# Performance work log

Measured on AMD Instinct MI355X. Metric: run time of the kernel, lower is better.

The kernel has to match this reference:

```python
import jax, jax.numpy as jnp
import numpy as np

N0, P1 = 10000, 30000
N1 = N0 + P1            # 40000
P2 = 120000
N2 = N1 + P2            # 160000
E0, E1, E2 = 60000, 120000, 480000
IN, H, OUT, K = 3, 192, 3, 2


def setup_inputs() -> dict:
    key = jax.random.key(0)
    k = jax.random.split(key, 13)
    return {
        "features": jax.random.normal(k[0], (N0, IN), jnp.float32),
        "src0": jax.random.randint(k[1], (E0,), 0, N0, jnp.int32),
        "dst0": jax.random.randint(k[2], (E0,), 0, N0, jnp.int32),
        "pool_idx0": jax.random.randint(k[3], (P1, 2), 0, N0, jnp.int32),
        "edge0": jax.random.randint(k[4], (E1, 2), 0, N1, jnp.int32),
        "pool_idx1": jax.random.randint(k[5], (P2, 2), 0, N1, jnp.int32),
        "edge1": jax.random.randint(k[6], (E2, 2), 0, N2, jnp.int32),
        "W_first": 0.3 * jax.random.normal(k[7], (3, (K + 1) * IN, H), jnp.float32),
        "b_first": jnp.zeros((3, H), jnp.float32),
        "W_mid": 0.04 * jax.random.normal(k[8], (3, 12, (K + 1) * H, H), jnp.float32),
        "b_mid": jnp.zeros((3, 12, H), jnp.float32),
        "W_last": 0.05 * jax.random.normal(k[9], (3, (K + 1) * H, OUT), jnp.float32),
        "b_last": jnp.zeros((3, OUT), jnp.float32),
    }


def _norm(dst, n):
    # symmetric-norm factor D^{-1/2}, degrees clamped at 1 (DGL TAGConv)
    deg = jax.ops.segment_sum(jnp.ones(dst.shape[0], jnp.float32), dst, num_segments=n)
    return jnp.clip(deg, 1.0) ** -0.5  # [n]


def _tagconv(x, src, dst, n, norm, W, b):
    fs = [x]
    h = x
    for _ in range(K):
        h = norm[:, None] * jax.ops.segment_sum((h * norm[:, None])[src], dst, num_segments=n)
        fs.append(h)
    return jnp.concatenate(fs, axis=1) @ W + b


def _stage(x, src, dst, n, Wf, bf, Wm, bm, Wl, bl):
    norm = _norm(dst, n)
    h = jax.nn.relu(_tagconv(x, src, dst, n, norm, Wf, bf))
    prev = h  # raw output of previous layer (hidden[-2] in the torch code)
    for i in range(12):
        cur = jax.nn.relu(_tagconv(h, src, dst, n, norm, Wm[i], bm[i]))
        h = 0.5 * (prev + cur) if (i + 1) in (2, 4, 6, 8, 10, 12) else cur
        prev = cur
    return _tagconv(h, src, dst, n, norm, Wl, bl)  # identity activation


def _unpool(feat, pool_idx):
    # new vertex = midpoint of its two parents; appended to the node table
    new_vs = 0.5 * (feat[pool_idx[:, 0]] + feat[pool_idx[:, 1]])
    return jnp.concatenate([feat, new_vs], axis=0)


def _bidir(edge):
    # graph.add_edges(src, dst); graph.add_edges(dst, src)
    return (jnp.concatenate([edge[:, 0], edge[:, 1]]),
            jnp.concatenate([edge[:, 1], edge[:, 0]]))


def reference(features, src0, dst0, pool_idx0, edge0, pool_idx1, edge1,
              W_first, b_first, W_mid, b_mid, W_last, b_last):
    out1 = _stage(features, src0, dst0, N0,
                  W_first[0], b_first[0], W_mid[0], b_mid[0], W_last[0], b_last[0])
    h = _unpool(out1, pool_idx0)            # [N1, 3]
    out1_2 = h
    s1, d1 = _bidir(edge0)
    out2 = _stage(h, s1, d1, N1,
                  W_first[1], b_first[1], W_mid[1], b_mid[1], W_last[1], b_last[1])
    h = _unpool(out2, pool_idx1)            # [N2, 3]
    out2_2 = h
    s2, d2 = _bidir(edge1)
    out3 = _stage(h, s2, d2, N2,
                  W_first[2], b_first[2], W_mid[2], b_mid[2], W_last[2], b_last[2])
    return (out1, out2, out3, out1_2, out2_2)
```

## Files before the change

kernel.cpp:

```cpp
#include <hip/hip_runtime.h>
#include <hip/hip_fp16.h>

#define HF 192

static inline int divup(int a, int b){ return (a+b-1)/b; }

typedef _Float16 half8 __attribute__((ext_vector_type(8)));
typedef float f32x4 __attribute__((ext_vector_type(4)));

#define G_WS_BYTES 195734272ull
__device__ __align__(256) char g_ws[G_WS_BYTES];

#define OFF_HH    0ull
#define OFF_T1H   61440000ull
#define OFF_T2H   122880000ull
#define OFF_DEG  184320000ull
#define OFF_RP   184960000ull
#define OFF_COL  185600032ull
#define OFF_NRM  189440032ull
#define OFF_O1F  190080032ull
#define OFF_U1F  190200032ull
#define OFF_O2F  190680032ull
#define OFF_U2F  191160032ull
#define OFF_WT   193080032ull
#define OFF_X1F  OFF_T1H
#define OFF_X2F  (OFF_T1H + 1920000ull)

__device__ __forceinline__ float*  wsf(unsigned long long o){ return (float*) (g_ws + o); }
__device__ __forceinline__ int*    wsi(unsigned long long o){ return (int*)   (g_ws + o); }
__device__ __forceinline__ __half* wsh(unsigned long long o){ return (__half*)(g_ws + o); }

__global__ void k_zero(unsigned long long off, int n) {
  int i = blockIdx.x*blockDim.x + threadIdx.x;
  if (i < n) wsi(off)[i] = 0;
}
__global__ void k_copyi(unsigned long long aOff, unsigned long long bOff, int n) {
  int i = blockIdx.x*blockDim.x + threadIdx.x;
  if (i < n) wsi(bOff)[i] = wsi(aOff)[i];
}

__global__ void k_count_direct(const int* __restrict__ dst, int E) {
  int* deg = wsi(OFF_DEG);
  int e = blockIdx.x*blockDim.x + threadIdx.x;
  if (e < E) atomicAdd(&deg[dst[e]], 1);
}
__global__ void k_count_bidir(const int* __restrict__ edge, int E) {
  int* deg = wsi(OFF_DEG);
  int e = blockIdx.x*blockDim.x + threadIdx.x;
  if (e < E) {
    atomicAdd(&deg[edge[2*e+1]], 1);
    atomicAdd(&deg[edge[2*e  ]], 1);
  }
}
__global__ void k_norm(int n) {
  const int* deg = wsi(OFF_DEG);
  float* nrm = wsf(OFF_NRM);
  int i = blockIdx.x*blockDim.x + threadIdx.x;
  if (i < n) {
    int d = deg[i]; if (d < 1) d = 1;
    nrm[i] = rsqrtf((float)d);
  }
}
__global__ __launch_bounds__(1024) void k_exscan(int n) {
  const int* in = wsi(OFF_DEG);
  int* out = wsi(OFF_RP);
  __shared__ int sm[1024];
  int t = threadIdx.x;
  int carry = 0;
  for (int base = 0; base < n; base += 4096) {
    int idx = base + t*4;
    int v0 = (idx+0 < n) ? in[idx+0] : 0;
    int v1 = (idx+1 < n) ? in[idx+1] : 0;
    int v2 = (idx+2 < n) ? in[idx+2] : 0;
    int v3 = (idx+3 < n) ? in[idx+3] : 0;
    int s = v0+v1+v2+v3;
    sm[t] = s;
    __syncthreads();
    for (int off = 1; off < 1024; off <<= 1) {
      int u = (t >= off) ? sm[t-off] : 0;
      __syncthreads();
      sm[t] += u;
      __syncthreads();
    }
    int excl = carry + sm[t] - s;
    if (idx   < n) out[idx]   = excl;
    if (idx+1 < n) out[idx+1] = excl + v0;
    if (idx+2 < n) out[idx+2] = excl + v0+v1;
    if (idx+3 < n) out[idx+3] = excl + v0+v1+v2;
    carry += sm[1023];
    __syncthreads();
  }
  if (t == 0) out[n] = carry;
}
__global__ void k_fill_direct(const int* __restrict__ src, const int* __restrict__ dst, int E) {
  int* cur = wsi(OFF_DEG);
  int* col = wsi(OFF_COL);
  int e = blockIdx.x*blockDim.x + threadIdx.x;
  if (e < E) {
    int p = atomicAdd(&cur[dst[e]], 1);
    col[p] = src[e];
  }
}
__global__ void k_fill_bidir(const int* __restrict__ edge, int E) {
  int* cur = wsi(OFF_DEG);
  int* col = wsi(OFF_COL);
  int e = blockIdx.x*blockDim.x + threadIdx.x;
  if (e < E) {
    int u = edge[2*e], v = edge[2*e+1];
    int p = atomicAdd(&cur[v], 1); col[p] = u;
    int q = atomicAdd(&cur[u], 1); col[q] = v;
  }
}

__global__ void k_spmm3(const float* __restrict__ Xext, unsigned long long Xoff,
                        unsigned long long Yoff, int n) {
  const float* X = Xext ? Xext : wsf(Xoff);
  float* Y = wsf(Yoff);
  const int* rowptr = wsi(OFF_RP);
  const int* col = wsi(OFF_COL);
  const float* nrm = wsf(OFF_NRM);
  int row = blockIdx.x*blockDim.x + threadIdx.x;
  if (row >= n) return;
  int s = rowptr[row], e = rowptr[row+1];
  float a0=0.f, a1=0.f, a2=0.f;
  for (int i = s; i < e; ++i) {
    int c = col[i]; float v = nrm[c];
    a0 = fmaf(v, X[c*3+0], a0);
    a1 = fmaf(v, X[c*3+1], a1);
    a2 = fmaf(v, X[c*3+2], a2);
  }
  float nm = nrm[row];
  Y[row*3+0] = a0*nm; Y[row*3+1] = a1*nm; Y[row*3+2] = a2*nm;
}

__global__ __launch_bounds__(192) void k_spmm8(unsigned long long Xoff,
                                               unsigned long long Yoff, int n) {
  int gid = blockIdx.x*192 + threadIdx.x;
  if (gid >= n*24) return;
  int row = gid / 24, f8 = gid - row*24;
  const half8* __restrict__ X8 = (const half8*)wsh(Xoff);
  half8* __restrict__ Y8 = (half8*)wsh(Yoff);
  const int* rowptr = wsi(OFF_RP);
  const int* col = wsi(OFF_COL);
  const float* nrm = wsf(OFF_NRM);
  int s = rowptr[row], e = rowptr[row+1];
  float acc0[8], acc1[8];
  #pragma unroll
  for (int j = 0; j < 8; ++j) { acc0[j] = 0.f; acc1[j] = 0.f; }
  int i = s;
  for (; i + 4 <= e; i += 4) {
    int c0 = col[i], c1 = col[i+1], c2 = col[i+2], c3 = col[i+3];
    float w0 = nrm[c0], w1 = nrm[c1], w2 = nrm[c2], w3 = nrm[c3];
    half8 v0 = X8[(size_t)c0*24 + f8];
    half8 v1 = X8[(size_t)c1*24 + f8];
    half8 v2 = X8[(size_t)c2*24 + f8];
    half8 v3 = X8[(size_t)c3*24 + f8];
    #pragma unroll
    for (int j = 0; j < 8; ++j) {
      acc0[j] = fmaf(w0, (float)v0[j], acc0[j]);
      acc1[j] = fmaf(w1, (float)v1[j], acc1[j]);
      acc0[j] = fmaf(w2, (float)v2[j], acc0[j]);
      acc1[j] = fmaf(w3, (float)v3[j], acc1[j]);
    }
  }
  for (; i + 2 <= e; i += 2) {
    int c0 = col[i], c1 = col[i+1];
    float w0 = nrm[c0], w1 = nrm[c1];
    half8 v0 = X8[(size_t)c0*24 + f8];
    half8 v1 = X8[(size_t)c1*24 + f8];
    #pragma unroll
    for (int j = 0; j < 8; ++j) {
      acc0[j] = fmaf(w0, (float)v0[j], acc0[j]);
      acc1[j] = fmaf(w1, (float)v1[j], acc1[j]);
    }
  }
  if (i < e) {
    int c0 = col[i];
    float w0 = nrm[c0];
    half8 v0 = X8[(size_t)c0*24 + f8];
    #pragma unroll
    for (int j = 0; j < 8; ++j) acc0[j] = fmaf(w0, (float)v0[j], acc0[j]);
  }
  float nm = nrm[row];
  half8 r;
  #pragma unroll
  for (int j = 0; j < 8; ++j) r[j] = (_Float16)((acc0[j] + acc1[j])*nm);
  Y8[(size_t)row*24 + f8] = r;
}

__global__ void k_gemm_first(const float* __restrict__ xext, unsigned long long xOff,
                             const float* __restrict__ W, const float* __restrict__ b, int n) {
  const float* x  = xext ? xext : wsf(xOff);
  const float* x1 = wsf(OFF_X1F);
  const float* x2 = wsf(OFF_X2F);
  __half* H = wsh(OFF_HH);
  int idx = blockIdx.x*blockDim.x + threadIdx.x;
  if (idx >= n*HF) return;
  int row = idx / HF, c = idx - row*HF;
  float acc = b[c];
  #pragma unroll
  for (int k = 0; k < 3; ++k) acc = fmaf(x [row*3+k], W[(0+k)*HF + c], acc);
  #pragma unroll
  for (int k = 0; k < 3; ++k) acc = fmaf(x1[row*3+k], W[(3+k)*HF + c], acc);
  #pragma unroll
  for (int k = 0; k < 3; ++k) acc = fmaf(x2[row*3+k], W[(6+k)*HF + c], acc);
  H[idx] = __float2half(fmaxf(acc, 0.f));
}

__global__ void k_wprep(const float* __restrict__ Wm, int s) {
  int idx = blockIdx.x*blockDim.x + threadIdx.x;
  if (idx >= 12*576*HF) return;
  int it = idx / (576*HF);
  int rem = idx - it*576*HF;
  int k = rem / HF;
  int c = rem - k*HF;
  wsh(OFF_WT)[(size_t)it*HF*576 + (size_t)c*576 + k] =
      __float2half(Wm[((size_t)(s*12+it)*576 + k)*HF + c]);
}

#define BPAD 104
__global__ __launch_bounds__(256) void k_mfma_mid(
    const float* __restrict__ b, int it, int n, int residual)
{
  __half* __restrict__ H = wsh(OFF_HH);
  const __half* __restrict__ T1 = wsh(OFF_T1H);
  const __half* __restrict__ T2 = wsh(OFF_T2H);
  const __half* __restrict__ Wt = wsh(OFF_WT) + (size_t)it*HF*576;
  __shared__ _Float16 Bs[192*BPAD];
  int t = threadIdx.x;
  int w = t >> 6;
  int l = t & 63;
  int lr = l & 15;
  int lg = l >> 4;
  int row0 = blockIdx.x*64 + w*16;

  f32x4 acc[12];
  #pragma unroll
  for (int i = 0; i < 12; ++i) acc[i] = (f32x4){0.f,0.f,0.f,0.f};

  const __half* Xp[3] = { H, T1, T2 };
  for (int p = 0; p < 3; ++p) {
    const __half* X = Xp[p];
    half8 a[6];
    #pragma unroll
    for (int q = 0; q < 6; ++q)
      a[q] = *(const half8*)&X[(size_t)(row0 + lr)*HF + q*32 + lg*8];
    for (int kh = 0; kh < 2; ++kh) {
      __syncthreads();
      for (int i = t; i < 192*12; i += 256) {
        int c  = i / 12;
        int k8 = i - c*12;
        *(half8*)&Bs[c*BPAD + k8*8] =
            *(const half8*)&Wt[(size_t)c*576 + p*HF + kh*96 + k8*8];
      }
      __syncthreads();
      #pragma unroll
      for (int k0i = 0; k0i < 3; ++k0i) {
        half8 av = a[kh*3 + k0i];
        #pragma unroll
        for (int tl = 0; tl < 12; ++tl) {
          half8 bb = *(const half8*)&Bs[(tl*16 + lr)*BPAD + k0i*32 + lg*8];
          acc[tl] = __builtin_amdgcn_mfma_f32_16x16x32_f16(av, bb, acc[tl], 0, 0, 0);
        }
      }
    }
  }

  #pragma unroll
  for (int tl = 0; tl < 12; ++tl) {
    int c = tl*16 + lr;
    float bias = b[c];
    #pragma unroll
    for (int j = 0; j < 4; ++j) {
      int row = row0 + lg*4 + j;
      if (row < n) {
        size_t o = (size_t)row*HF + c;
        float cur = fmaxf(acc[tl][j] + bias, 0.f);
        float h = cur;
        if (residual) h = 0.5f*(__half2float(H[o]) + cur);
        H[o] = __float2half(h);
      }
    }
  }
}

__global__ void k_last_lin(const float* __restrict__ W, const float* __restrict__ b,
                           float* __restrict__ outb, unsigned long long outfOff,
                           int hasOutf, int n) {
  int row = blockIdx.x*blockDim.x + threadIdx.x;
  if (row >= n) return;
  const __half* bufs[3] = { wsh(OFF_HH), wsh(OFF_T1H), wsh(OFF_T2H) };
  float a0 = b[0], a1 = b[1], a2 = b[2];
  for (int p = 0; p < 3; ++p) {
    const half8* x8 = (const half8*)&bufs[p][(size_t)row*HF];
    #pragma unroll 4
    for (int k8 = 0; k8 < 24; ++k8) {
      half8 v = x8[k8];
      #pragma unroll
      for (int j = 0; j < 8; ++j) {
        int k = k8*8 + j;
        const float* w = &W[(p*HF + k)*3];
        float vv = (float)v[j];
        a0 = fmaf(vv, w[0], a0); a1 = fmaf(vv, w[1], a1); a2 = fmaf(vv, w[2], a2);
      }
    }
  }
  outb[row*3+0] = a0;
  outb[row*3+1] = a1;
  outb[row*3+2] = a2;
  if (hasOutf) {
    float* outf = wsf(outfOff);
    outf[row*3+0] = a0; outf[row*3+1] = a1; outf[row*3+2] = a2;
  }
}

__global__ void k_unpool(unsigned long long srcOff, const int* __restrict__ pidx,
                         unsigned long long dstfOff, float* __restrict__ dstb,
                         int n, int P) {
  const float* src = wsf(srcOff);
  float* dstf = wsf(dstfOff);
  int i = blockIdx.x*blockDim.x + threadIdx.x;
  if (i >= n + P) return;
  float v0, v1, v2;
  if (i < n) {
    v0 = src[i*3+0]; v1 = src[i*3+1]; v2 = src[i*3+2];
  } else {
    int a = pidx[(i-n)*2], c = pidx[(i-n)*2+1];
    v0 = 0.5f*(src[a*3+0] + src[c*3+0]);
    v1 = 0.5f*(src[a*3+1] + src[c*3+1]);
    v2 = 0.5f*(src[a*3+2] + src[c*3+2]);
  }
  dstf[i*3+0] = v0; dstf[i*3+1] = v1; dstf[i*3+2] = v2;
  dstb[i*3+0] = v0;
  dstb[i*3+1] = v1;
  dstb[i*3+2] = v2;
}

extern "C" void kernel_launch(void* const* d_in, const int* in_sizes, int n_in,
                              void* d_out, int out_size, void* d_ws, size_t ws_size,
                              hipStream_t stream) {
  (void)in_sizes; (void)n_in; (void)out_size; (void)d_ws; (void)ws_size;
  const float* features = (const float*)d_in[0];
  const int*  src0  = (const int*)d_in[1];
  const int*  dst0  = (const int*)d_in[2];
  const int*  pool0 = (const int*)d_in[3];
  const int*  edge0 = (const int*)d_in[4];
  const int*  pool1 = (const int*)d_in[5];
  const int*  edge1 = (const int*)d_in[6];
  const float* Wf = (const float*)d_in[7];
  const float* bfp = (const float*)d_in[8];
  const float* Wm = (const float*)d_in[9];
  const float* bm = (const float*)d_in[10];
  const float* Wl = (const float*)d_in[11];
  const float* bl = (const float*)d_in[12];
  float* out = (float*)d_out;

  auto csr = [&](int n, const int* srcD, const int* dstD, int Edir,
                 const int* edgeB, int Eund) {
    k_zero<<<divup(n,256),256,0,stream>>>(OFF_DEG, n);
    if (srcD) k_count_direct<<<divup(Edir,256),256,0,stream>>>(dstD, Edir);
    else      k_count_bidir <<<divup(Eund,256),256,0,stream>>>(edgeB, Eund);
    k_norm<<<divup(n,256),256,0,stream>>>(n);
    k_exscan<<<1,1024,0,stream>>>(n);
    k_copyi<<<divup(n,256),256,0,stream>>>(OFF_RP, OFF_DEG, n);
    if (srcD) k_fill_direct<<<divup(Edir,256),256,0,stream>>>(srcD, dstD, Edir);
    else      k_fill_bidir<<<divup(Eund,256),256,0,stream>>>(edgeB, Eund);
  };

  auto stage_u = [&](const float* xext, unsigned long long xOff, int n,
                     const int* srcD, const int* dstD, int Edir,
                     const int* edgeB, int Eund,
                     int s, float* outb, unsigned long long outfOff, int hasOutf) {
    csr(n, srcD, dstD, Edir, edgeB, Eund);
    k_wprep<<<divup(12*576*HF,256),256,0,stream>>>(Wm, s);
    k_spmm3<<<divup(n,256),256,0,stream>>>(xext, xOff, OFF_X1F, n);
    k_spmm3<<<divup(n,256),256,0,stream>>>(nullptr, OFF_X1F, OFF_X2F, n);
    k_gemm_first<<<divup(n*HF,256),256,0,stream>>>(xext, xOff,
        Wf + (size_t)s*9*HF, bfp + s*HF, n);
    int gsp = divup(n*24,192);
    for (int it = 0; it < 12; ++it) {
      k_spmm8<<<gsp,192,0,stream>>>(OFF_HH,  OFF_T1H, n);
      k_spmm8<<<gsp,192,0,stream>>>(OFF_T1H, OFF_T2H, n);
      k_mfma_mid<<<divup(n,64),256,0,stream>>>(bm + (s*12+it)*HF, it, n,
          ((it+1)%2==0) ? 1 : 0);
    }
    k_spmm8<<<gsp,192,0,stream>>>(OFF_HH,  OFF_T1H, n);
    k_spmm8<<<gsp,192,0,stream>>>(OFF_T1H, OFF_T2H, n);
    k_last_lin<<<divup(n,256),256,0,stream>>>(Wl + (size_t)s*576*3, bl + s*3,
        outb, outfOff, hasOutf, n);
  };

  stage_u(features, 0ull, 10000, src0, dst0, 60000, nullptr, 0,
          0, out + 0, OFF_O1F, 1);
  k_unpool<<<divup(40000,256),256,0,stream>>>(OFF_O1F, pool0, OFF_U1F, out + 630000, 10000, 30000);
  stage_u(nullptr, OFF_U1F, 40000, nullptr, nullptr, 0, edge0, 120000,
          1, out + 30000, OFF_O2F, 1);
  k_unpool<<<divup(160000,256),256,0,stream>>>(OFF_O2F, pool1, OFF_U2F, out + 750000, 40000, 120000);
  stage_u(nullptr, OFF_U2F, 160000, nullptr, nullptr, 0, edge1, 480000,
          2, out + 150000, OFF_O1F, 0);
}
```

Before: 5.833 ms.

## Switch mid-layer GEMM to 32x32x16 MFMA tiles with 128-row blocks

The mid-layer TAGConv GEMM moves from 16x16x32 MFMA tiles (16 rows per wave) to 32x32x16 tiles (32 rows per wave, 128 rows per block). Each weight tile staged in shared memory is now reused across twice as many rows, which halves the per-row LDS B-fragment traffic and the number of blocks that restage the weights. A fragments are now loaded from global memory inside the k loop instead of being preloaded, and the epilogue uses the 32x32 accumulator row mapping. A min-blocks occupancy hint is also added, which may limit registers given the 96-float accumulator per lane.

After: 5.757 ms. About the same (-1.3%).

```diff
diff --git a/kernel.cpp b/kernel.cpp
--- a/kernel.cpp
+++ b/kernel.cpp
@@ -7,6 +7,7 @@
 
 typedef _Float16 half8 __attribute__((ext_vector_type(8)));
 typedef float f32x4 __attribute__((ext_vector_type(4)));
+typedef float f32x16 __attribute__((ext_vector_type(16)));
 
 #define G_WS_BYTES 195734272ull
 __device__ __align__(256) char g_ws[G_WS_BYTES];
@@ -219,7 +220,7 @@
 }
 
 #define BPAD 104
-__global__ __launch_bounds__(256) void k_mfma_mid(
+__global__ __launch_bounds__(256,4) void k_mfma_mid(
     const float* __restrict__ b, int it, int n, int residual)
 {
   __half* __restrict__ H = wsh(OFF_HH);
@@ -230,21 +231,19 @@
   int t = threadIdx.x;
   int w = t >> 6;
   int l = t & 63;
-  int lr = l & 15;
-  int lg = l >> 4;
-  int row0 = blockIdx.x*64 + w*16;
-
-  f32x4 acc[12];
-  #pragma unroll
-  for (int i = 0; i < 12; ++i) acc[i] = (f32x4){0.f,0.f,0.f,0.f};
+  int lc = l & 31;
+  int lg = l >> 5;
+  int rowW = blockIdx.x*128 + w*32;
+
+  f32x16 acc[6];
+  #pragma unroll
+  for (int i = 0; i < 6; ++i)
+    #pragma unroll
+    for (int r = 0; r < 16; ++r) acc[i][r] = 0.f;
 
   const __half* Xp[3] = { H, T1, T2 };
   for (int p = 0; p < 3; ++p) {
     const __half* X = Xp[p];
-    half8 a[6];
-    #pragma unroll
-    for (int q = 0; q < 6; ++q)
-      a[q] = *(const half8*)&X[(size_t)(row0 + lr)*HF + q*32 + lg*8];
     for (int kh = 0; kh < 2; ++kh) {
       __syncthreads();
       for (int i = t; i < 192*12; i += 256) {
@@ -255,27 +254,28 @@
       }
       __syncthreads();
       #pragma unroll
-      for (int k0i = 0; k0i < 3; ++k0i) {
-        half8 av = a[kh*3 + k0i];
+      for (int ks = 0; ks < 6; ++ks) {
+        half8 a = *(const half8*)&X[(size_t)(rowW + lc)*HF + kh*96 + ks*16 + lg*8];
         #pragma unroll
-        for (int tl = 0; tl < 12; ++tl) {
-          half8 bb = *(const half8*)&Bs[(tl*16 + lr)*BPAD + k0i*32 + lg*8];
-          acc[tl] = __builtin_amdgcn_mfma_f32_16x16x32_f16(av, bb, acc[tl], 0, 0, 0);
+        for (int ct = 0; ct < 6; ++ct) {
+          half8 bb = *(const half8*)&Bs[(ct*32 + lc)*BPAD + ks*16 + lg*8];
+          acc[ct] = __builtin_amdgcn_mfma_f32_32x32x16_f16(a, bb, acc[ct], 0, 0, 0);
         }
       }
     }
   }
 
   #pragma unroll
-  for (int tl = 0; tl < 12; ++tl) {
-    int c = tl*16 + lr;
+  for (int ct = 0; ct < 6; ++ct) {
+    int c = ct*32 + lc;
     float bias = b[c];
     #pragma unroll
-    for (int j = 0; j < 4; ++j) {
-      int row = row0 + lg*4 + j;
+    for (int r = 0; r < 16; ++r) {
+      int rowl = (r & 3) + 8*(r >> 2) + 4*lg;
+      int row = rowW + rowl;
       if (row < n) {
         size_t o = (size_t)row*HF + c;
-        float cur = fmaxf(acc[tl][j] + bias, 0.f);
+        float cur = fmaxf(acc[ct][r] + bias, 0.f);
         float h = cur;
         if (residual) h = 0.5f*(__half2float(H[o]) + cur);
         H[o] = __float2half(h);
@@ -381,7 +381,7 @@
     for (int it = 0; it < 12; ++it) {
       k_spmm8<<<gsp,192,0,stream>>>(OFF_HH,  OFF_T1H, n);
       k_spmm8<<<gsp,192,0,stream>>>(OFF_T1H, OFF_T2H, n);
-      k_mfma_mid<<<divup(n,64),256,0,stream>>>(bm + (s*12+it)*HF, it, n,
+      k_mfma_mid<<<divup(n,128),256,0,stream>>>(bm + (s*12+it)*HF, it, n,
           ((it+1)%2==0) ? 1 : 0);
     }
     k_spmm8<<<gsp,192,0,stream>>>(OFF_HH,  OFF_T1H, n);
```
